# Kernel optimization log

Hardware: AMD Instinct MI355X
Metric: run time of the kernel (lower is better)

Reference implementation:

```python
import jax, jax.numpy as jnp
import numpy as np


def _conv(x, kernel):
    # x: [N, C, H, W], kernel: [O, I, kh, kw]; torch conv2d padding=1 (symmetric both dims)
    return jax.lax.conv_general_dilated(
        x, kernel, window_strides=(1, 1), padding=((1, 1), (1, 1)),
        dimension_numbers=("NCHW", "OIHW", "NCHW"))


def setup_inputs() -> dict:
    key = jax.random.key(0)
    k1, k2 = jax.random.split(key)
    shape = (2, 7, 7, 3, 256, 256)  # bs, ah, aw, c, h, w
    infer = jax.random.normal(k1, shape, dtype=jnp.float32)
    ref = jax.random.normal(k2, shape, dtype=jnp.float32)
    return {"infer": infer, "ref": ref}


def reference(infer, ref):
    bs, ah, aw, c, h, w = infer.shape
    x = infer.reshape(bs * ah * aw, c, h, w)
    y = ref.reshape(bs * ah * aw, c, h, w)
    # fixed gradient kernels, identical across all 3x3 in/out channel pairs
    kh = jnp.broadcast_to(
        jnp.array([-0.5, 0.0, 0.5], jnp.float32).reshape(1, 1, 1, 3), (3, 3, 1, 3))
    kv = jnp.broadcast_to(
        jnp.array([-0.5, 0.0, 0.5], jnp.float32).reshape(1, 1, 3, 1), (3, 3, 3, 1))
    # torch padding=1 on a (1,3) kernel -> output (h+2, w); on (3,1) -> (h, w+2)
    loss_h = jnp.mean(jnp.abs(_conv(x, kh) - _conv(y, kh)))
    loss_v = jnp.mean(jnp.abs(_conv(x, kv) - _conv(y, kv)))
    return (loss_h + loss_v) / 2.0
```

## Files before the change

kernel.cpp:

```cpp
#include <hip/hip_runtime.h>


#define W 256
#define NIMG 98
#define CH_STRIDE 65536
#define TH 8
#define HALO (TH + 2)
#define NSTRIP 32
#define NBLK (NIMG * NSTRIP)
#define SCALE (0.25f / 6472704.0f)

__device__ __forceinline__ void async_copy16(const float* g, float* l) {
  __builtin_amdgcn_global_load_lds(
      (const __attribute__((address_space(1))) void*)g,
      (__attribute__((address_space(3))) void*)l,
      16, 0, 0);
}

struct SmemT {
  float raw[6][HALO][W];
  float Dsh[HALO][W];
  float ws[4];
};

__device__ __forceinline__ float block_body(const float* __restrict__ x,
                                            const float* __restrict__ y,
                                            SmemT& sm) {
  const int tid   = threadIdx.x;
  const int lane  = tid & 63;
  const int wv    = tid >> 6;
  const int b     = blockIdx.x;
  const int n     = b >> 5;
  const int strip = b & 31;
  const int r0    = strip * TH;

  const float* xb = x + (size_t)n * 3 * CH_STRIDE;
  const float* yb = y + (size_t)n * 3 * CH_STRIDE;

  #pragma unroll
  for (int i = 0; i < 15; ++i) {
    const int id = wv + 4 * i;
    const int s  = id / HALO;
    const int lr = id % HALO;
    int g = r0 - 1 + lr;
    g = (g < 0) ? 0 : (g > 255 ? 255 : g);
    const float* gp = ((s < 3) ? (xb + s * CH_STRIDE) : (yb + (s - 3) * CH_STRIDE))
                      + g * W + (lane << 2);
    async_copy16(gp, &sm.raw[s][lr][0]);
  }
  __syncthreads();

  const int w = tid;
  float d[HALO];
  #pragma unroll
  for (int lr = 0; lr < HALO; ++lr) {
    const int g = r0 - 1 + lr;
    float v = 0.f;
    if (g >= 0 && g < 256) {
      v = (sm.raw[0][lr][w] - sm.raw[3][lr][w])
        + (sm.raw[1][lr][w] - sm.raw[4][lr][w])
        + (sm.raw[2][lr][w] - sm.raw[5][lr][w]);
    }
    d[lr] = v;
    sm.Dsh[lr][w] = v;
  }
  __syncthreads();

  float acc = 0.f;
  #pragma unroll
  for (int r = 0; r < TH; ++r) {
    const float* rp = sm.Dsh[r + 1];
    float left  = (w > 0)     ? rp[w - 1] : 0.f;
    float right = (w < W - 1) ? rp[w + 1] : 0.f;
    acc += fabsf(right - left) + fabsf(d[r + 2] - d[r]);
  }

  #pragma unroll
  for (int off = 32; off > 0; off >>= 1)
    acc += __shfl_down(acc, off, 64);
  if (lane == 0) sm.ws[wv] = acc;
  __syncthreads();
  return sm.ws[0] + sm.ws[1] + sm.ws[2] + sm.ws[3];
}

__global__ __launch_bounds__(256) void detail_stage1(
    const float* __restrict__ x, const float* __restrict__ y,
    float* __restrict__ partial) {
  __shared__ SmemT sm;
  float s = block_body(x, y, sm);
  if (threadIdx.x == 0) partial[blockIdx.x] = s;
}

__global__ __launch_bounds__(256) void detail_stage1_atomic(
    const float* __restrict__ x, const float* __restrict__ y,
    float* __restrict__ out) {
  __shared__ SmemT sm;
  float s = block_body(x, y, sm);
  if (threadIdx.x == 0) atomicAdd(out, s * SCALE);
}

__global__ __launch_bounds__(256) void detail_stage2(
    const float* __restrict__ partial, float* __restrict__ out) {
  float acc = 0.f;
  for (int i = threadIdx.x; i < NBLK; i += 256) acc += partial[i];
  #pragma unroll
  for (int off = 32; off > 0; off >>= 1)
    acc += __shfl_down(acc, off, 64);
  __shared__ float ws[4];
  if ((threadIdx.x & 63) == 0) ws[threadIdx.x >> 6] = acc;
  __syncthreads();
  if (threadIdx.x == 0) out[0] = (ws[0] + ws[1] + ws[2] + ws[3]) * SCALE;
}

extern "C" void kernel_launch(void* const* d_in, const int* in_sizes, int n_in,
                              void* d_out, int out_size, void* d_ws, size_t ws_size,
                              hipStream_t stream) {
  const float* infer = (const float*)d_in[0];
  const float* ref   = (const float*)d_in[1];
  float* out = (float*)d_out;

  if (ws_size >= NBLK * sizeof(float)) {
    float* partial = (float*)d_ws;
    detail_stage1<<<NBLK, 256, 0, stream>>>(infer, ref, partial);
    detail_stage2<<<1, 256, 0, stream>>>(partial, out);
  } else {
    hipMemsetAsync(out, 0, sizeof(float), stream);
    detail_stage1_atomic<<<NBLK, 256, 0, stream>>>(infer, ref, out);
  }
}
```

Measured before the change: 168.9 us.

## Replace LDS staging with register-streamed rows and wavefront shuffles

Each block becomes a single 64-lane wavefront. Every lane loads float4 columns straight into registers, and the loop software-pipelines one row ahead. The old async global-to-LDS copy, the shared diff buffer and both block barriers are gone. Horizontal neighbours now come from lane shuffles, and the vertical gradient uses a rolling three-row register window. The block count stays the same with fewer threads per block, so load latency must be hidden by many small blocks in flight rather than by one bulk async copy.

```diff
diff --git a/kernel.cpp b/kernel.cpp
--- a/kernel.cpp
+++ b/kernel.cpp
@@ -5,97 +5,93 @@
 #define NIMG 98
 #define CH_STRIDE 65536
 #define TH 8
-#define HALO (TH + 2)
 #define NSTRIP 32
 #define NBLK (NIMG * NSTRIP)
 #define SCALE (0.25f / 6472704.0f)
 
-__device__ __forceinline__ void async_copy16(const float* g, float* l) {
-  __builtin_amdgcn_global_load_lds(
-      (const __attribute__((address_space(1))) void*)g,
-      (__attribute__((address_space(3))) void*)l,
-      16, 0, 0);
+struct Row6 { float4 a0, a1, a2, b0, b1, b2; };
+
+__device__ __forceinline__ int clampg(int g) {
+  return g < 0 ? 0 : (g > 255 ? 255 : g);
 }
 
-struct SmemT {
-  float raw[6][HALO][W];
-  float Dsh[HALO][W];
-  float ws[4];
-};
+__device__ __forceinline__ Row6 issue_row(const float* __restrict__ xb,
+                                          const float* __restrict__ yb,
+                                          int g) {
+  const int ro = g * W;
+  Row6 r;
+  r.a0 = *(const float4*)(xb + ro);
+  r.a1 = *(const float4*)(xb + ro + CH_STRIDE);
+  r.a2 = *(const float4*)(xb + ro + 2 * CH_STRIDE);
+  r.b0 = *(const float4*)(yb + ro);
+  r.b1 = *(const float4*)(yb + ro + CH_STRIDE);
+  r.b2 = *(const float4*)(yb + ro + 2 * CH_STRIDE);
+  return r;
+}
 
-__device__ __forceinline__ float block_body(const float* __restrict__ x,
-                                            const float* __restrict__ y,
-                                            SmemT& sm) {
-  const int tid   = threadIdx.x;
-  const int lane  = tid & 63;
-  const int wv    = tid >> 6;
+__device__ __forceinline__ float4 combine(const Row6& r, float m) {
+  float4 d;
+  d.x = m * ((r.a0.x - r.b0.x) + (r.a1.x - r.b1.x) + (r.a2.x - r.b2.x));
+  d.y = m * ((r.a0.y - r.b0.y) + (r.a1.y - r.b1.y) + (r.a2.y - r.b2.y));
+  d.z = m * ((r.a0.z - r.b0.z) + (r.a1.z - r.b1.z) + (r.a2.z - r.b2.z));
+  d.w = m * ((r.a0.w - r.b0.w) + (r.a1.w - r.b1.w) + (r.a2.w - r.b2.w));
+  return d;
+}
+
+__device__ __forceinline__ float band_body(const float* __restrict__ x,
+                                           const float* __restrict__ y) {
+  const int lane  = threadIdx.x;
   const int b     = blockIdx.x;
   const int n     = b >> 5;
   const int strip = b & 31;
   const int r0    = strip * TH;
 
-  const float* xb = x + (size_t)n * 3 * CH_STRIDE;
-  const float* yb = y + (size_t)n * 3 * CH_STRIDE;
+  const float* xb = x + (size_t)n * 3 * CH_STRIDE + (lane << 2);
+  const float* yb = y + (size_t)n * 3 * CH_STRIDE + (lane << 2);
 
-  #pragma unroll
-  for (int i = 0; i < 15; ++i) {
-    const int id = wv + 4 * i;
-    const int s  = id / HALO;
-    const int lr = id % HALO;
-    int g = r0 - 1 + lr;
-    g = (g < 0) ? 0 : (g > 255 ? 255 : g);
-    const float* gp = ((s < 3) ? (xb + s * CH_STRIDE) : (yb + (s - 3) * CH_STRIDE))
-                      + g * W + (lane << 2);
-    async_copy16(gp, &sm.raw[s][lr][0]);
-  }
-  __syncthreads();
+  Row6 s0 = issue_row(xb, yb, clampg(r0 - 1));
+  Row6 s1 = issue_row(xb, yb, r0);
+  Row6 pend = issue_row(xb, yb, r0 + 1);
 
-  const int w = tid;
-  float d[HALO];
-  #pragma unroll
-  for (int lr = 0; lr < HALO; ++lr) {
-    const int g = r0 - 1 + lr;
-    float v = 0.f;
-    if (g >= 0 && g < 256) {
-      v = (sm.raw[0][lr][w] - sm.raw[3][lr][w])
-        + (sm.raw[1][lr][w] - sm.raw[4][lr][w])
-        + (sm.raw[2][lr][w] - sm.raw[5][lr][w]);
-    }
-    d[lr] = v;
-    sm.Dsh[lr][w] = v;
-  }
-  __syncthreads();
+  float4 dprev = combine(s0, (r0 - 1 >= 0) ? 1.f : 0.f);
+  float4 dcur  = combine(s1, 1.f);
 
   float acc = 0.f;
   #pragma unroll
   for (int r = 0; r < TH; ++r) {
-    const float* rp = sm.Dsh[r + 1];
-    float left  = (w > 0)     ? rp[w - 1] : 0.f;
-    float right = (w < W - 1) ? rp[w + 1] : 0.f;
-    acc += fabsf(right - left) + fabsf(d[r + 2] - d[r]);
+    Row6 nxt = issue_row(xb, yb, clampg(r0 + r + 2));
+    float4 dnext = combine(pend, (r0 + r + 1 <= 255) ? 1.f : 0.f);
+
+    float lm = __shfl_up(dcur.w, 1);
+    if (lane == 0) lm = 0.f;
+    float rp = __shfl_down(dcur.x, 1);
+    if (lane == 63) rp = 0.f;
+    acc += fabsf(dcur.y - lm) + fabsf(dcur.z - dcur.x)
+         + fabsf(dcur.w - dcur.y) + fabsf(rp - dcur.z);
+
+    acc += fabsf(dnext.x - dprev.x) + fabsf(dnext.y - dprev.y)
+         + fabsf(dnext.z - dprev.z) + fabsf(dnext.w - dprev.w);
+
+    dprev = dcur; dcur = dnext; pend = nxt;
   }
 
   #pragma unroll
   for (int off = 32; off > 0; off >>= 1)
     acc += __shfl_down(acc, off, 64);
-  if (lane == 0) sm.ws[wv] = acc;
-  __syncthreads();
-  return sm.ws[0] + sm.ws[1] + sm.ws[2] + sm.ws[3];
+  return acc;
 }
 
-__global__ __launch_bounds__(256) void detail_stage1(
+__global__ __launch_bounds__(64) void detail_stage1(
     const float* __restrict__ x, const float* __restrict__ y,
     float* __restrict__ partial) {
-  __shared__ SmemT sm;
-  float s = block_body(x, y, sm);
+  float s = band_body(x, y);
   if (threadIdx.x == 0) partial[blockIdx.x] = s;
 }
 
-__global__ __launch_bounds__(256) void detail_stage1_atomic(
+__global__ __launch_bounds__(64) void detail_stage1_atomic(
     const float* __restrict__ x, const float* __restrict__ y,
     float* __restrict__ out) {
-  __shared__ SmemT sm;
-  float s = block_body(x, y, sm);
+  float s = band_body(x, y);
   if (threadIdx.x == 0) atomicAdd(out, s * SCALE);
 }
 
@@ -121,10 +117,10 @@
 
   if (ws_size >= NBLK * sizeof(float)) {
     float* partial = (float*)d_ws;
-    detail_stage1<<<NBLK, 256, 0, stream>>>(infer, ref, partial);
+    detail_stage1<<<NBLK, 64, 0, stream>>>(infer, ref, partial);
     detail_stage2<<<1, 256, 0, stream>>>(partial, out);
   } else {
     hipMemsetAsync(out, 0, sizeof(float), stream);
-    detail_stage1_atomic<<<NBLK, 256, 0, stream>>>(infer, ref, out);
+    detail_stage1_atomic<<<NBLK, 64, 0, stream>>>(infer, ref, out);
   }
 }
```

Result: no change. 171.5 us (+1.6%).

## Give each wave its own row band with double-buffered async row streaming

Applied to the files above, without the earlier changes.

Each wave now owns a full 8-row band and streams the 10 halo rows through a two-slot LDS buffer, issuing async global-to-LDS copies for a later row while combining the current one. Horizontal neighbours come from lane shuffles on float4 values, so the shared D buffer and block-wide barriers go away. Block indices are swizzled across the 8 XCDs. The aim is to overlap loads with compute and cut LDS use, which should raise occupancy. The cost is hand-managed vmcnt/lgkmcnt waits that could be fragile if the compiler reorders memory operations.

```diff
diff --git a/kernel.cpp b/kernel.cpp
--- a/kernel.cpp
+++ b/kernel.cpp
@@ -5,9 +5,10 @@
 #define NIMG 98
 #define CH_STRIDE 65536
 #define TH 8
-#define HALO (TH + 2)
-#define NSTRIP 32
-#define NBLK (NIMG * NSTRIP)
+#define NBAND (NIMG * 32)
+#define WAVES_PER_BLK 4
+#define NBLK (NBAND / WAVES_PER_BLK)
+#define NXCD 8
 #define SCALE (0.25f / 6472704.0f)
 
 __device__ __forceinline__ void async_copy16(const float* g, float* l) {
@@ -17,63 +18,106 @@
       16, 0, 0);
 }
 
+#define WAITVM6() asm volatile("s_waitcnt vmcnt(6)" ::: "memory")
+#define WAITVM0() asm volatile("s_waitcnt vmcnt(0)" ::: "memory")
+#define WAITLGKM0() asm volatile("s_waitcnt lgkmcnt(0)" ::: "memory")
+
 struct SmemT {
-  float raw[6][HALO][W];
-  float Dsh[HALO][W];
-  float ws[4];
+  float raw[WAVES_PER_BLK][2][6][W];
+  float ws[WAVES_PER_BLK];
 };
+
+__device__ __forceinline__ float4 combine_slot(const float (*slot)[W],
+                                               int lane4, float m) {
+  const float4 a0 = *(const float4*)&slot[0][lane4];
+  const float4 a1 = *(const float4*)&slot[1][lane4];
+  const float4 a2 = *(const float4*)&slot[2][lane4];
+  const float4 b0 = *(const float4*)&slot[3][lane4];
+  const float4 b1 = *(const float4*)&slot[4][lane4];
+  const float4 b2 = *(const float4*)&slot[5][lane4];
+  float4 d;
+  d.x = m * ((a0.x - b0.x) + (a1.x - b1.x) + (a2.x - b2.x));
+  d.y = m * ((a0.y - b0.y) + (a1.y - b1.y) + (a2.y - b2.y));
+  d.z = m * ((a0.z - b0.z) + (a1.z - b1.z) + (a2.z - b2.z));
+  d.w = m * ((a0.w - b0.w) + (a1.w - b1.w) + (a2.w - b2.w));
+  return d;
+}
 
 __device__ __forceinline__ float block_body(const float* __restrict__ x,
                                             const float* __restrict__ y,
                                             SmemT& sm) {
-  const int tid   = threadIdx.x;
-  const int lane  = tid & 63;
-  const int wv    = tid >> 6;
-  const int b     = blockIdx.x;
-  const int n     = b >> 5;
-  const int strip = b & 31;
+  const int tid  = threadIdx.x;
+  const int lane = tid & 63;
+  const int wv   = tid >> 6;
+  const int lane4 = lane << 2;
+
+  const int b    = blockIdx.x;
+  const int swz  = (b % NXCD) * (NBLK / NXCD) + b / NXCD;
+  const int band = swz * WAVES_PER_BLK + wv;
+  const int n     = band >> 5;
+  const int strip = band & 31;
   const int r0    = strip * TH;
 
-  const float* xb = x + (size_t)n * 3 * CH_STRIDE;
-  const float* yb = y + (size_t)n * 3 * CH_STRIDE;
+  const float* xb = x + (size_t)n * 3 * CH_STRIDE + lane4;
+  const float* yb = y + (size_t)n * 3 * CH_STRIDE + lane4;
 
-  #pragma unroll
-  for (int i = 0; i < 15; ++i) {
-    const int id = wv + 4 * i;
-    const int s  = id / HALO;
-    const int lr = id % HALO;
-    int g = r0 - 1 + lr;
-    g = (g < 0) ? 0 : (g > 255 ? 255 : g);
-    const float* gp = ((s < 3) ? (xb + s * CH_STRIDE) : (yb + (s - 3) * CH_STRIDE))
-                      + g * W + (lane << 2);
-    async_copy16(gp, &sm.raw[s][lr][0]);
-  }
-  __syncthreads();
-
-  const int w = tid;
-  float d[HALO];
-  #pragma unroll
-  for (int lr = 0; lr < HALO; ++lr) {
-    const int g = r0 - 1 + lr;
-    float v = 0.f;
-    if (g >= 0 && g < 256) {
-      v = (sm.raw[0][lr][w] - sm.raw[3][lr][w])
-        + (sm.raw[1][lr][w] - sm.raw[4][lr][w])
-        + (sm.raw[2][lr][w] - sm.raw[5][lr][w]);
-    }
-    d[lr] = v;
-    sm.Dsh[lr][w] = v;
-  }
-  __syncthreads();
+  #define STAGE(lr, slot) do {                                        \
+    int g_ = r0 - 1 + (lr);                                           \
+    g_ = (g_ < 0) ? 0 : (g_ > 255 ? 255 : g_);                        \
+    const float* gx_ = xb + g_ * W;                                   \
+    const float* gy_ = yb + g_ * W;                                   \
+    async_copy16(gx_,                  &sm.raw[wv][slot][0][0]);      \
+    async_copy16(gx_ + CH_STRIDE,      &sm.raw[wv][slot][1][0]);      \
+    async_copy16(gx_ + 2 * CH_STRIDE,  &sm.raw[wv][slot][2][0]);      \
+    async_copy16(gy_,                  &sm.raw[wv][slot][3][0]);      \
+    async_copy16(gy_ + CH_STRIDE,      &sm.raw[wv][slot][4][0]);      \
+    async_copy16(gy_ + 2 * CH_STRIDE,  &sm.raw[wv][slot][5][0]);      \
+  } while (0)
 
   float acc = 0.f;
-  #pragma unroll
-  for (int r = 0; r < TH; ++r) {
-    const float* rp = sm.Dsh[r + 1];
-    float left  = (w > 0)     ? rp[w - 1] : 0.f;
-    float right = (w < W - 1) ? rp[w + 1] : 0.f;
-    acc += fabsf(right - left) + fabsf(d[r + 2] - d[r]);
-  }
+  float4 dA, dB, dC;
+
+  #define ACCROW(Dm2, Dm1, Dc) do {                                   \
+    float lm_ = __shfl_up((Dm1).w, 1);                                \
+    if (lane == 0) lm_ = 0.f;                                         \
+    float rr_ = __shfl_down((Dm1).x, 1);                              \
+    if (lane == 63) rr_ = 0.f;                                        \
+    acc += fabsf((Dm1).y - lm_) + fabsf((Dm1).z - (Dm1).x)           \
+         + fabsf((Dm1).w - (Dm1).y) + fabsf(rr_ - (Dm1).z);          \
+    acc += fabsf((Dc).x - (Dm2).x) + fabsf((Dc).y - (Dm2).y)         \
+         + fabsf((Dc).z - (Dm2).z) + fabsf((Dc).w - (Dm2).w);        \
+  } while (0)
+
+  #define MASK(lr) (((lr) == 0) ? (r0 > 0 ? 1.f : 0.f)                \
+                  : ((lr) == 9) ? (r0 < 248 ? 1.f : 0.f) : 1.f)
+
+  STAGE(0, 0);
+  STAGE(1, 1);
+
+  #define ITER(k, Rm2, Rm1, Rc, DO_ACC, DO_ISSUE)                     \
+    do {                                                              \
+      if ((k) < 9) { WAITVM6(); } else { WAITVM0(); }                 \
+      Rc = combine_slot(sm.raw[wv][(k) & 1], lane4, MASK(k));         \
+      WAITLGKM0();                                                    \
+      if (DO_ISSUE) STAGE((k) + 2, (k) & 1);                          \
+      if (DO_ACC) ACCROW(Rm2, Rm1, Rc);                               \
+    } while (0)
+
+  ITER(0, dA, dA, dA, 0, 1);
+  ITER(1, dA, dA, dB, 0, 1);
+  ITER(2, dA, dB, dC, 1, 1);
+  ITER(3, dB, dC, dA, 1, 1);
+  ITER(4, dC, dA, dB, 1, 1);
+  ITER(5, dA, dB, dC, 1, 1);
+  ITER(6, dB, dC, dA, 1, 1);
+  ITER(7, dC, dA, dB, 1, 1);
+  ITER(8, dA, dB, dC, 1, 0);
+  ITER(9, dB, dC, dA, 1, 0);
+
+  #undef ITER
+  #undef MASK
+  #undef ACCROW
+  #undef STAGE
 
   #pragma unroll
   for (int off = 32; off > 0; off >>= 1)
```

Measured after the change: 172.8 us. +2.3%, slower.
